# Kernel optimization log

Hardware: AMD Instinct MI355X
Metric: run time of the kernel (lower is better)

The kernel has to match this reference:

```python
import jax, jax.numpy as jnp
import numpy as np

SCALE_H = 160.0
SCALE_W = 160.0
ALIGNED = False


def setup_inputs() -> dict:
    key = jax.random.key(0)
    k1, k2, k3, k4 = jax.random.split(key, 4)
    N, C, H, W, K = 8, 256, 160, 160, 1024
    feat = jax.random.normal(k1, (N, C, H, W), dtype=jnp.float32)
    b = jax.random.randint(k2, (K,), 0, N).astype(jnp.float32)
    xs = jnp.sort(jax.random.uniform(k3, (K, 2), dtype=jnp.float32), axis=1)
    ys = jnp.sort(jax.random.uniform(k4, (K, 2), dtype=jnp.float32), axis=1)
    rois = jnp.stack([b, xs[:, 0], ys[:, 0], xs[:, 1], ys[:, 1]], axis=1)
    return {"input_feature_map": feat, "rois": rois,
            "output_height": 14, "output_width": 14}


def _roi_align(feat, rois, output_height, output_width):
    N, C, H, W = feat.shape
    K = rois.shape[0]
    b = rois[:, 0].astype(jnp.int32)
    x1 = rois[:, 1] * SCALE_W
    y1 = rois[:, 2] * SCALE_H
    x2 = rois[:, 3] * SCALE_W
    y2 = rois[:, 4] * SCALE_H
    # normalized [0,1] grid over the ROI interior
    gx = jnp.linspace(0.0, 1.0, output_width, dtype=feat.dtype)
    gy = jnp.linspace(0.0, 1.0, output_height, dtype=feat.dtype)
    fx = x1[:, None, None] + gx[None, None, :] * (x2 - x1)[:, None, None]  # (K,1,Wo)
    fy = y1[:, None, None] + gy[None, :, None] * (y2 - y1)[:, None, None]  # (K,Ho,1)
    # convert to grid_sample normalized coords, then back to pixel coords
    if ALIGNED:
        ngx = fx / (W - 1) * 2 - 1
        ngy = fy / (H - 1) * 2 - 1
        ix = (ngx + 1) * 0.5 * (W - 1)
        iy = (ngy + 1) * 0.5 * (H - 1)
    else:
        ngx = fx / W * 2 - 1
        ngy = fy / H * 2 - 1
        ix = ((ngx + 1) * W - 1) * 0.5
        iy = ((ngy + 1) * H - 1) * 0.5
    x0 = jnp.floor(ix).astype(jnp.int32)
    y0 = jnp.floor(iy).astype(jnp.int32)
    x1i = x0 + 1
    y1i = y0 + 1
    wx1 = ix - x0.astype(feat.dtype)
    wx0 = 1.0 - wx1
    wy1 = iy - y0.astype(feat.dtype)
    wy0 = 1.0 - wy1
    # zeros padding: out-of-bounds corners contribute 0
    vx0 = ((x0 >= 0) & (x0 < W)).astype(feat.dtype)
    vx1 = ((x1i >= 0) & (x1i < W)).astype(feat.dtype)
    vy0 = ((y0 >= 0) & (y0 < H)).astype(feat.dtype)
    vy1 = ((y1i >= 0) & (y1i < H)).astype(feat.dtype)
    x0c = jnp.clip(x0, 0, W - 1)
    x1c = jnp.clip(x1i, 0, W - 1)
    y0c = jnp.clip(y0, 0, H - 1)
    y1c = jnp.clip(y1i, 0, H - 1)
    # flat gather table: (N*H*W, C) -- no per-ROI feature-map duplication
    featf = jnp.transpose(feat, (0, 2, 3, 1)).reshape(N * H * W, C)
    bb = b[:, None, None]  # (K,1,1)

    def corner(yy, xx, w):
        lin = (bb * H + yy) * W + xx  # broadcast -> (K,Ho,Wo)
        lin = jnp.broadcast_to(lin, (K, output_height, output_width))
        v = featf[lin.reshape(-1)].reshape(K, output_height, output_width, C)
        w = jnp.broadcast_to(w, (K, output_height, output_width))
        return v * w[..., None]

    out = (corner(y0c, x0c, wy0 * wx0 * vy0 * vx0)
           + corner(y0c, x1c, wy0 * wx1 * vy0 * vx1)
           + corner(y1c, x0c, wy1 * wx0 * vy1 * vx0)
           + corner(y1c, x1c, wy1 * wx1 * vy1 * vx1))
    return jnp.transpose(out, (0, 3, 1, 2))  # (K, C, Ho, Wo)


def reference(input_feature_map, rois, output_height, output_width):
    return _roi_align(input_feature_map, rois, int(output_height), int(output_width))
```

## Files before the change

### kernel.cpp

```cpp
#include <hip/hip_runtime.h>
#include <hip/hip_fp16.h>


#define FM_N 8
#define FM_C 256
#define FM_H 160
#define FM_W 160
#define PLANE (FM_H * FM_W)
#define PLANE4 (PLANE / 4)
#define OH 14
#define OW 14
#define OSP (OH * OW)
#define KMAX 1024
#define SCALE_HW 160.0f
#define MAIN_BLK 1024
#define ROWS 81
#define LDSW 164
#define ROW_F4 (FM_W / 4)
#define PL_PIX (ROWS * LDSW)
#define PL_F4 (ROWS * ROW_F4)
#define FRONTPAD 2
#define TAILPAD 6

typedef float f4 __attribute__((ext_vector_type(4)));

#define WS_KINFO_OFF 32
#define WS_SAMPLES_BYTE_OFF 12544

__device__ __forceinline__ float iy_of(float y1, float y2, int oy) {
  return fmaf((float)oy * (1.0f / (OH - 1)), y2 - y1, y1) - 0.5f;
}

__global__ __launch_bounds__(1024) void setup_kernel(
    const float* __restrict__ rois, int K, int* __restrict__ ws) {
  __shared__ int cnt[16];
  __shared__ int soff[16];
  const int t = threadIdx.x;
  if (t < 16) cnt[t] = 0;
  __syncthreads();
  int posA = 0, posB = 0, c0 = 0, b = 0;
  if (t < K) {
    b = (int)rois[t * 5];
    const float y1 = rois[t * 5 + 2] * SCALE_HW;
    const float y2 = rois[t * 5 + 4] * SCALE_HW;
#pragma unroll
    for (int oy = 0; oy < OH; ++oy)
      c0 += (iy_of(y1, y2, oy) < 80.0f) ? 1 : 0;
    posA = atomicAdd(&cnt[b * 2 + 0], c0 * OW);
    posB = atomicAdd(&cnt[b * 2 + 1], (OH - c0) * OW);
  }
  __syncthreads();
  if (t == 0) {
    int acc = 0;
    for (int i = 0; i < 16; ++i) { soff[i] = acc; acc += cnt[i]; }
  }
  __syncthreads();
  if (t < 16) { ws[t] = cnt[t]; ws[16 + t] = soff[t]; }
  if (t < K) {
    ws[WS_KINFO_OFF + 3 * t + 0] = soff[b * 2 + 0] + posA;
    ws[WS_KINFO_OFF + 3 * t + 1] = soff[b * 2 + 1] + posB;
    ws[WS_KINFO_OFF + 3 * t + 2] = c0;
  }
}

__global__ __launch_bounds__(256) void precompute_kernel(
    const float* __restrict__ rois, const int* __restrict__ ws, int total,
    uint4* __restrict__ samples) {
  const int g = blockIdx.x * 256 + threadIdx.x;
  if (g >= total) return;
  const int k = g / OSP;
  const int s = g - k * OSP;
  const int oy = s / OW;
  const int ox = s - oy * OW;

  const float x1 = rois[k * 5 + 1] * SCALE_HW;
  const float y1 = rois[k * 5 + 2] * SCALE_HW;
  const float x2 = rois[k * 5 + 3] * SCALE_HW;
  const float y2 = rois[k * 5 + 4] * SCALE_HW;

  const float ix = fmaf((float)ox * (1.0f / (OW - 1)), x2 - x1, x1) - 0.5f;
  const float iy = iy_of(y1, y2, oy);

  const float fx0 = floorf(ix);
  const float fy0 = floorf(iy);
  const int x0 = (int)fx0;
  const int y0 = (int)fy0;
  const float wx1 = ix - fx0;
  const float wy1 = iy - fy0;

  const bool vx0 = (x0 >= 0 && x0 < FM_W);
  const bool vx1 = (x0 + 1 >= 0 && x0 + 1 < FM_W);
  const unsigned vy0 = (y0 >= 0 && y0 < FM_H) ? 1u : 0u;
  const unsigned vy1 = (y0 + 1 >= 0 && y0 + 1 < FM_H) ? 1u : 0u;

  const int x0c = min(max(x0, 0), FM_W - 1);
  const int x1c = min(max(x0 + 1, 0), FM_W - 1);
  const int y0c = min(max(y0, 0), FM_H - 1);
  const int y1c = min(max(y0 + 1, 0), FM_H - 1);

  const int ca = ws[WS_KINFO_OFF + 3 * k + 0];
  const int cb = ws[WS_KINFO_OFF + 3 * k + 1];
  const int c0 = ws[WS_KINFO_OFF + 3 * k + 2];
  const int h = (oy >= c0) ? 1 : 0;
  const int row0 = h ? 79 : 0;

  const int yl0 = y0c - row0;
  const int o00 = yl0 * LDSW + x0c;
  const int o01 = yl0 * LDSW + x1c;
  const int bx = vx1 ? (o01 - 1) : o00;
  const unsigned bxs = (unsigned)(bx + FRONTPAD);
  const unsigned dyr = (unsigned)(y1c - y0c);
  unsigned wq = (unsigned)(wy1 * 8192.0f + 0.5f);
  wq = wq > 8191u ? 8191u : wq;

  const __half2 axh = __floats2half2_rn((1.0f - wx1) * (vx0 ? 1.0f : 0.0f),
                                        wx1 * (vx1 ? 1.0f : 0.0f));
  uint4 sd;
  sd.x = bxs | (dyr << 15) | (wq << 16) | (vy0 << 29) | (vy1 << 30);
  sd.y = *(const unsigned*)&axh;
  sd.z = (unsigned)(k * (FM_C * OSP) + s);
  sd.w = 0;

  const int pos = h ? (cb + (oy - c0) * OW + ox) : (ca + oy * OW + ox);
  samples[pos] = sd;
}

__global__ __launch_bounds__(MAIN_BLK) void roi_align_main_kernel(
    const float* __restrict__ feat, const int* __restrict__ ws,
    const uint4* __restrict__ samples, float* __restrict__ out) {
  __shared__ __align__(16) uint2 planeBuf[FRONTPAD + PL_PIX + TAILPAD];

  const int q = blockIdx.x;
  const int b = blockIdx.y;
  const int h = blockIdx.z;
  const int t = threadIdx.x;
  const int row0 = h ? 79 : 0;
  const int c0ch = 4 * q;

  const int scount = ws[b * 2 + h];
  const int soff = ws[16 + b * 2 + h];
  const uint4* __restrict__ stream = samples + soff;

  const uint2 zz = {0u, 0u};
  if (t < FRONTPAD) planeBuf[t] = zz;
  if (t < TAILPAD) planeBuf[FRONTPAD + PL_PIX + t] = zz;
  if (t < ROWS * 4) {
    const int y = t >> 2;
    planeBuf[FRONTPAD + y * LDSW + FM_W + (t & 3)] = zz;
  }

  {
    const f4* __restrict__ s0 =
        (const f4*)(feat + ((size_t)b * FM_C + c0ch) * PLANE) + row0 * ROW_F4;
    const f4* __restrict__ s1 = s0 + PLANE4;
    const f4* __restrict__ s2 = s0 + 2 * PLANE4;
    const f4* __restrict__ s3 = s0 + 3 * PLANE4;
    for (int i = t; i < PL_F4; i += MAIN_BLK) {
      const f4 a = __builtin_nontemporal_load(&s0[i]);
      const f4 bb = __builtin_nontemporal_load(&s1[i]);
      const f4 c = __builtin_nontemporal_load(&s2[i]);
      const f4 d = __builtin_nontemporal_load(&s3[i]);
      const int y = (int)((unsigned)i / ROW_F4);
      const int j = i - y * ROW_F4;
      const __half2 p0l = __floats2half2_rn(a.x, bb.x);
      const __half2 p0h = __floats2half2_rn(c.x, d.x);
      const __half2 p1l = __floats2half2_rn(a.y, bb.y);
      const __half2 p1h = __floats2half2_rn(c.y, d.y);
      const __half2 p2l = __floats2half2_rn(a.z, bb.z);
      const __half2 p2h = __floats2half2_rn(c.z, d.z);
      const __half2 p3l = __floats2half2_rn(a.w, bb.w);
      const __half2 p3h = __floats2half2_rn(c.w, d.w);
      uint4 u01, u23;
      u01.x = *(const unsigned*)&p0l;
      u01.y = *(const unsigned*)&p0h;
      u01.z = *(const unsigned*)&p1l;
      u01.w = *(const unsigned*)&p1h;
      u23.x = *(const unsigned*)&p2l;
      u23.y = *(const unsigned*)&p2h;
      u23.z = *(const unsigned*)&p3l;
      u23.w = *(const unsigned*)&p3h;
      uint4* __restrict__ dst =
          (uint4*)&planeBuf[FRONTPAD + y * LDSW + 4 * j];
      dst[0] = u01;
      dst[1] = u23;
    }
  }
  __syncthreads();

  const uint2* __restrict__ pb = planeBuf;
  float* __restrict__ outc = out + (size_t)c0ch * OSP;
#pragma unroll 2
  for (int w = t; w < scount; w += MAIN_BLK) {
    const uint4 sd = stream[w];
    const int bxs = (int)(sd.x & 0x7FFFu);
    const int o10 = bxs + (int)((sd.x >> 15) & 1u) * LDSW;

    const uint2 L0 = pb[bxs];
    const uint2 R0 = pb[bxs + 1];
    const uint2 L1 = pb[o10];
    const uint2 R1 = pb[o10 + 1];

    const __half2 ax = *(const __half2*)&sd.y;
    const __half2 axl = __half2half2(__low2half(ax));
    const __half2 axr = __half2half2(__high2half(ax));

    const __half2 hx0l = __hfma2(*(const __half2*)&R0.x, axr,
                                 __hmul2(*(const __half2*)&L0.x, axl));
    const __half2 hx0h = __hfma2(*(const __half2*)&R0.y, axr,
                                 __hmul2(*(const __half2*)&L0.y, axl));
    const __half2 hx1l = __hfma2(*(const __half2*)&R1.x, axr,
                                 __hmul2(*(const __half2*)&L1.x, axl));
    const __half2 hx1h = __hfma2(*(const __half2*)&R1.y, axr,
                                 __hmul2(*(const __half2*)&L1.y, axl));

    const float wy1 = (float)((sd.x >> 16) & 0x1FFFu) * (1.0f / 8192.0f);
    const float ay0 = ((sd.x >> 29) & 1u) ? (1.0f - wy1) : 0.0f;
    const float ay1 = ((sd.x >> 30) & 1u) ? wy1 : 0.0f;

    const float vA = ay0 * __low2float(hx0l) + ay1 * __low2float(hx1l);
    const float vB = ay0 * __high2float(hx0l) + ay1 * __high2float(hx1l);
    const float vC = ay0 * __low2float(hx0h) + ay1 * __low2float(hx1h);
    const float vD = ay0 * __high2float(hx0h) + ay1 * __high2float(hx1h);

    float* __restrict__ dst = outc + sd.z;
    dst[0] = vA;
    dst[OSP] = vB;
    dst[2 * OSP] = vC;
    dst[3 * OSP] = vD;
  }
}

extern "C" void kernel_launch(void* const* d_in, const int* in_sizes, int n_in,
                              void* d_out, int out_size, void* d_ws, size_t ws_size,
                              hipStream_t stream) {
  const float* feat = (const float*)d_in[0];
  const float* rois = (const float*)d_in[1];
  float* out = (float*)d_out;
  int* ws = (int*)d_ws;
  uint4* samples = (uint4*)((char*)d_ws + WS_SAMPLES_BYTE_OFF);

  const int K = in_sizes[1] / 5;
  const int total = K * OSP;

  setup_kernel<<<1, 1024, 0, stream>>>(rois, K, ws);
  precompute_kernel<<<(total + 255) / 256, 256, 0, stream>>>(rois, ws, total,
                                                             samples);
  roi_align_main_kernel<<<dim3(FM_C / 4, FM_N, 2), MAIN_BLK, 0, stream>>>(
      feat, ws, samples, out);
}
```

Before: 91.24 us.

## Tile feature map into row quarters with eight channels per block

Measured after the change: 97.67 us. +7.0%, slower.

```diff
diff --git a/kernel.cpp b/kernel.cpp
--- a/kernel.cpp
+++ b/kernel.cpp
@@ -14,52 +14,67 @@
 #define KMAX 1024
 #define SCALE_HW 160.0f
 #define MAIN_BLK 1024
-#define ROWS 81
+#define QROWS 40
+#define ROWS 41
 #define LDSW 164
 #define ROW_F4 (FM_W / 4)
 #define PL_PIX (ROWS * LDSW)
-#define PL_F4 (ROWS * ROW_F4)
-#define FRONTPAD 2
-#define TAILPAD 6
+#define FRONTPAD 1
+#define TAILPAD 4
 
 typedef float f4 __attribute__((ext_vector_type(4)));
 
-#define WS_KINFO_OFF 32
-#define WS_SAMPLES_BYTE_OFF 12544
+#define WS_KINFO_OFF 64
+#define WS_SAMPLES_BYTE_OFF 33024
 
 __device__ __forceinline__ float iy_of(float y1, float y2, int oy) {
   return fmaf((float)oy * (1.0f / (OH - 1)), y2 - y1, y1) - 0.5f;
 }
 
+__device__ __forceinline__ int quarter_of(float y1, float y2, int oy) {
+  const int y0 = (int)floorf(iy_of(y1, y2, oy));
+  const int y0c = min(max(y0, 0), FM_H - 1);
+  return y0c / QROWS;
+}
+
 __global__ __launch_bounds__(1024) void setup_kernel(
     const float* __restrict__ rois, int K, int* __restrict__ ws) {
-  __shared__ int cnt[16];
-  __shared__ int soff[16];
+  __shared__ int cnt[32];
+  __shared__ int soff[32];
   const int t = threadIdx.x;
-  if (t < 16) cnt[t] = 0;
-  __syncthreads();
-  int posA = 0, posB = 0, c0 = 0, b = 0;
+  if (t < 32) cnt[t] = 0;
+  __syncthreads();
+  int n[4] = {0, 0, 0, 0};
+  int st[4] = {0, 0, 0, 0};
+  int pos[4] = {0, 0, 0, 0};
+  int b = 0;
   if (t < K) {
     b = (int)rois[t * 5];
     const float y1 = rois[t * 5 + 2] * SCALE_HW;
     const float y2 = rois[t * 5 + 4] * SCALE_HW;
 #pragma unroll
-    for (int oy = 0; oy < OH; ++oy)
-      c0 += (iy_of(y1, y2, oy) < 80.0f) ? 1 : 0;
-    posA = atomicAdd(&cnt[b * 2 + 0], c0 * OW);
-    posB = atomicAdd(&cnt[b * 2 + 1], (OH - c0) * OW);
+    for (int oy = 0; oy < OH; ++oy) {
+      const int q = quarter_of(y1, y2, oy);
+      if (n[q] == 0) st[q] = oy;
+      n[q]++;
+    }
+#pragma unroll
+    for (int q = 0; q < 4; ++q)
+      if (n[q]) pos[q] = atomicAdd(&cnt[b * 4 + q], n[q] * OW);
   }
   __syncthreads();
   if (t == 0) {
     int acc = 0;
-    for (int i = 0; i < 16; ++i) { soff[i] = acc; acc += cnt[i]; }
-  }
-  __syncthreads();
-  if (t < 16) { ws[t] = cnt[t]; ws[16 + t] = soff[t]; }
+    for (int i = 0; i < 32; ++i) { soff[i] = acc; acc += cnt[i]; }
+  }
+  __syncthreads();
+  if (t < 32) { ws[t] = cnt[t]; ws[32 + t] = soff[t]; }
   if (t < K) {
-    ws[WS_KINFO_OFF + 3 * t + 0] = soff[b * 2 + 0] + posA;
-    ws[WS_KINFO_OFF + 3 * t + 1] = soff[b * 2 + 1] + posB;
-    ws[WS_KINFO_OFF + 3 * t + 2] = c0;
+#pragma unroll
+    for (int q = 0; q < 4; ++q) {
+      ws[WS_KINFO_OFF + 8 * t + q] = soff[b * 4 + q] + pos[q];
+      ws[WS_KINFO_OFF + 8 * t + 4 + q] = st[q];
+    }
   }
 }
 
@@ -98,11 +113,8 @@
   const int y0c = min(max(y0, 0), FM_H - 1);
   const int y1c = min(max(y0 + 1, 0), FM_H - 1);
 
-  const int ca = ws[WS_KINFO_OFF + 3 * k + 0];
-  const int cb = ws[WS_KINFO_OFF + 3 * k + 1];
-  const int c0 = ws[WS_KINFO_OFF + 3 * k + 2];
-  const int h = (oy >= c0) ? 1 : 0;
-  const int row0 = h ? 79 : 0;
+  const int q = y0c / QROWS;
+  const int row0 = q * QROWS;
 
   const int yl0 = y0c - row0;
   const int o00 = yl0 * LDSW + x0c;
@@ -121,27 +133,28 @@
   sd.z = (unsigned)(k * (FM_C * OSP) + s);
   sd.w = 0;
 
-  const int pos = h ? (cb + (oy - c0) * OW + ox) : (ca + oy * OW + ox);
-  samples[pos] = sd;
+  const int coff = ws[WS_KINFO_OFF + 8 * k + q];
+  const int stq = ws[WS_KINFO_OFF + 8 * k + 4 + q];
+  samples[coff + (oy - stq) * OW + ox] = sd;
 }
 
 __global__ __launch_bounds__(MAIN_BLK) void roi_align_main_kernel(
     const float* __restrict__ feat, const int* __restrict__ ws,
     const uint4* __restrict__ samples, float* __restrict__ out) {
-  __shared__ __align__(16) uint2 planeBuf[FRONTPAD + PL_PIX + TAILPAD];
-
-  const int q = blockIdx.x;
+  __shared__ __align__(16) uint4 planeBuf[FRONTPAD + PL_PIX + TAILPAD];
+
+  const int o8 = blockIdx.x;
   const int b = blockIdx.y;
-  const int h = blockIdx.z;
+  const int q = blockIdx.z;
   const int t = threadIdx.x;
-  const int row0 = h ? 79 : 0;
-  const int c0ch = 4 * q;
-
-  const int scount = ws[b * 2 + h];
-  const int soff = ws[16 + b * 2 + h];
+  const int row0 = q * QROWS;
+  const int c0ch = 8 * o8;
+
+  const int scount = ws[b * 4 + q];
+  const int soff = ws[32 + b * 4 + q];
   const uint4* __restrict__ stream = samples + soff;
 
-  const uint2 zz = {0u, 0u};
+  const uint4 zz = {0u, 0u, 0u, 0u};
   if (t < FRONTPAD) planeBuf[t] = zz;
   if (t < TAILPAD) planeBuf[FRONTPAD + PL_PIX + t] = zz;
   if (t < ROWS * 4) {
@@ -150,44 +163,36 @@
   }
 
   {
-    const f4* __restrict__ s0 =
-        (const f4*)(feat + ((size_t)b * FM_C + c0ch) * PLANE) + row0 * ROW_F4;
-    const f4* __restrict__ s1 = s0 + PLANE4;
-    const f4* __restrict__ s2 = s0 + 2 * PLANE4;
-    const f4* __restrict__ s3 = s0 + 3 * PLANE4;
-    for (int i = t; i < PL_F4; i += MAIN_BLK) {
-      const f4 a = __builtin_nontemporal_load(&s0[i]);
-      const f4 bb = __builtin_nontemporal_load(&s1[i]);
-      const f4 c = __builtin_nontemporal_load(&s2[i]);
-      const f4 d = __builtin_nontemporal_load(&s3[i]);
+    const f4* __restrict__ sp =
+        (const f4*)(feat + ((size_t)b * FM_C + c0ch) * PLANE);
+    for (int i = t; i < ROWS * ROW_F4; i += MAIN_BLK) {
       const int y = (int)((unsigned)i / ROW_F4);
       const int j = i - y * ROW_F4;
-      const __half2 p0l = __floats2half2_rn(a.x, bb.x);
-      const __half2 p0h = __floats2half2_rn(c.x, d.x);
-      const __half2 p1l = __floats2half2_rn(a.y, bb.y);
-      const __half2 p1h = __floats2half2_rn(c.y, d.y);
-      const __half2 p2l = __floats2half2_rn(a.z, bb.z);
-      const __half2 p2h = __floats2half2_rn(c.z, d.z);
-      const __half2 p3l = __floats2half2_rn(a.w, bb.w);
-      const __half2 p3h = __floats2half2_rn(c.w, d.w);
-      uint4 u01, u23;
-      u01.x = *(const unsigned*)&p0l;
-      u01.y = *(const unsigned*)&p0h;
-      u01.z = *(const unsigned*)&p1l;
-      u01.w = *(const unsigned*)&p1h;
-      u23.x = *(const unsigned*)&p2l;
-      u23.y = *(const unsigned*)&p2h;
-      u23.z = *(const unsigned*)&p3l;
-      u23.w = *(const unsigned*)&p3h;
-      uint4* __restrict__ dst =
-          (uint4*)&planeBuf[FRONTPAD + y * LDSW + 4 * j];
-      dst[0] = u01;
-      dst[1] = u23;
+      const int srow = min(row0 + y, FM_H - 1);
+      const int so = srow * ROW_F4 + j;
+      f4 v[8];
+#pragma unroll
+      for (int c = 0; c < 8; ++c)
+        v[c] = __builtin_nontemporal_load(&sp[c * PLANE4 + so]);
+      uint4* __restrict__ dst = &planeBuf[FRONTPAD + y * LDSW + 4 * j];
+#pragma unroll
+      for (int e = 0; e < 4; ++e) {
+        const __half2 a0 = __floats2half2_rn(v[0][e], v[1][e]);
+        const __half2 a1 = __floats2half2_rn(v[2][e], v[3][e]);
+        const __half2 a2 = __floats2half2_rn(v[4][e], v[5][e]);
+        const __half2 a3 = __floats2half2_rn(v[6][e], v[7][e]);
+        uint4 u;
+        u.x = *(const unsigned*)&a0;
+        u.y = *(const unsigned*)&a1;
+        u.z = *(const unsigned*)&a2;
+        u.w = *(const unsigned*)&a3;
+        dst[e] = u;
+      }
     }
   }
   __syncthreads();
 
-  const uint2* __restrict__ pb = planeBuf;
+  const uint4* __restrict__ pb = planeBuf;
   float* __restrict__ outc = out + (size_t)c0ch * OSP;
 #pragma unroll 2
   for (int w = t; w < scount; w += MAIN_BLK) {
@@ -195,38 +200,45 @@
     const int bxs = (int)(sd.x & 0x7FFFu);
     const int o10 = bxs + (int)((sd.x >> 15) & 1u) * LDSW;
 
-    const uint2 L0 = pb[bxs];
-    const uint2 R0 = pb[bxs + 1];
-    const uint2 L1 = pb[o10];
-    const uint2 R1 = pb[o10 + 1];
+    const uint4 L0 = pb[bxs];
+    const uint4 R0 = pb[bxs + 1];
+    const uint4 L1 = pb[o10];
+    const uint4 R1 = pb[o10 + 1];
 
     const __half2 ax = *(const __half2*)&sd.y;
     const __half2 axl = __half2half2(__low2half(ax));
     const __half2 axr = __half2half2(__high2half(ax));
 
-    const __half2 hx0l = __hfma2(*(const __half2*)&R0.x, axr,
-                                 __hmul2(*(const __half2*)&L0.x, axl));
-    const __half2 hx0h = __hfma2(*(const __half2*)&R0.y, axr,
-                                 __hmul2(*(const __half2*)&L0.y, axl));
-    const __half2 hx1l = __hfma2(*(const __half2*)&R1.x, axr,
-                                 __hmul2(*(const __half2*)&L1.x, axl));
-    const __half2 hx1h = __hfma2(*(const __half2*)&R1.y, axr,
-                                 __hmul2(*(const __half2*)&L1.y, axl));
+    const __half2 h0a = __hfma2(*(const __half2*)&R0.x, axr,
+                                __hmul2(*(const __half2*)&L0.x, axl));
+    const __half2 h0b = __hfma2(*(const __half2*)&R0.y, axr,
+                                __hmul2(*(const __half2*)&L0.y, axl));
+    const __half2 h0c = __hfma2(*(const __half2*)&R0.z, axr,
+                                __hmul2(*(const __half2*)&L0.z, axl));
+    const __half2 h0d = __hfma2(*(const __half2*)&R0.w, axr,
+                                __hmul2(*(const __half2*)&L0.w, axl));
+    const __half2 h1a = __hfma2(*(const __half2*)&R1.x, axr,
+                                __hmul2(*(const __half2*)&L1.x, axl));
+    const __half2 h1b = __hfma2(*(const __half2*)&R1.y, axr,
+                                __hmul2(*(const __half2*)&L1.y, axl));
+    const __half2 h1c = __hfma2(*(const __half2*)&R1.z, axr,
+                                __hmul2(*(const __half2*)&L1.z, axl));
+    const __half2 h1d = __hfma2(*(const __half2*)&R1.w, axr,
+                                __hmul2(*(const __half2*)&L1.w, axl));
 
     const float wy1 = (float)((sd.x >> 16) & 0x1FFFu) * (1.0f / 8192.0f);
     const float ay0 = ((sd.x >> 29) & 1u) ? (1.0f - wy1) : 0.0f;
     const float ay1 = ((sd.x >> 30) & 1u) ? wy1 : 0.0f;
 
-    const float vA = ay0 * __low2float(hx0l) + ay1 * __low2float(hx1l);
-    const float vB = ay0 * __high2float(hx0l) + ay1 * __high2float(hx1l);
-    const float vC = ay0 * __low2float(hx0h) + ay1 * __low2float(hx1h);
-    const float vD = ay0 * __high2float(hx0h) + ay1 * __high2float(hx1h);
-
     float* __restrict__ dst = outc + sd.z;
-    dst[0] = vA;
-    dst[OSP] = vB;
-    dst[2 * OSP] = vC;
-    dst[3 * OSP] = vD;
+    dst[0 * OSP] = ay0 * __low2float(h0a) + ay1 * __low2float(h1a);
+    dst[1 * OSP] = ay0 * __high2float(h0a) + ay1 * __high2float(h1a);
+    dst[2 * OSP] = ay0 * __low2float(h0b) + ay1 * __low2float(h1b);
+    dst[3 * OSP] = ay0 * __high2float(h0b) + ay1 * __high2float(h1b);
+    dst[4 * OSP] = ay0 * __low2float(h0c) + ay1 * __low2float(h1c);
+    dst[5 * OSP] = ay0 * __high2float(h0c) + ay1 * __high2float(h1c);
+    dst[6 * OSP] = ay0 * __low2float(h0d) + ay1 * __low2float(h1d);
+    dst[7 * OSP] = ay0 * __high2float(h0d) + ay1 * __high2float(h1d);
   }
 }
 
@@ -245,6 +257,6 @@
   setup_kernel<<<1, 1024, 0, stream>>>(rois, K, ws);
   precompute_kernel<<<(total + 255) / 256, 256, 0, stream>>>(rois, ws, total,
                                                              samples);
-  roi_align_main_kernel<<<dim3(FM_C / 4, FM_N, 2), MAIN_BLK, 0, stream>>>(
+  roi_align_main_kernel<<<dim3(FM_C / 8, FM_N, 4), MAIN_BLK, 0, stream>>>(
       feat, ws, samples, out);
 }
```

## Split feature plane into four row bands to shrink LDS tile and raise occupancy

Applied to the files above, without the earlier changes.

Result: slower. 95.86 us (+5.1%).

```diff
diff --git a/kernel.cpp b/kernel.cpp
--- a/kernel.cpp
+++ b/kernel.cpp
@@ -14,52 +14,67 @@
 #define KMAX 1024
 #define SCALE_HW 160.0f
 #define MAIN_BLK 1024
-#define ROWS 81
+#define QROWS 40
+#define ROWS 41
 #define LDSW 164
 #define ROW_F4 (FM_W / 4)
 #define PL_PIX (ROWS * LDSW)
-#define PL_F4 (ROWS * ROW_F4)
 #define FRONTPAD 2
 #define TAILPAD 6
 
 typedef float f4 __attribute__((ext_vector_type(4)));
 
-#define WS_KINFO_OFF 32
-#define WS_SAMPLES_BYTE_OFF 12544
+#define WS_KINFO_OFF 64
+#define WS_SAMPLES_BYTE_OFF 33024
 
 __device__ __forceinline__ float iy_of(float y1, float y2, int oy) {
   return fmaf((float)oy * (1.0f / (OH - 1)), y2 - y1, y1) - 0.5f;
 }
 
+__device__ __forceinline__ int quarter_of(float y1, float y2, int oy) {
+  const int y0 = (int)floorf(iy_of(y1, y2, oy));
+  const int y0c = min(max(y0, 0), FM_H - 1);
+  return y0c / QROWS;
+}
+
 __global__ __launch_bounds__(1024) void setup_kernel(
     const float* __restrict__ rois, int K, int* __restrict__ ws) {
-  __shared__ int cnt[16];
-  __shared__ int soff[16];
+  __shared__ int cnt[32];
+  __shared__ int soff[32];
   const int t = threadIdx.x;
-  if (t < 16) cnt[t] = 0;
-  __syncthreads();
-  int posA = 0, posB = 0, c0 = 0, b = 0;
+  if (t < 32) cnt[t] = 0;
+  __syncthreads();
+  int n[4] = {0, 0, 0, 0};
+  int st[4] = {0, 0, 0, 0};
+  int pos[4] = {0, 0, 0, 0};
+  int b = 0;
   if (t < K) {
     b = (int)rois[t * 5];
     const float y1 = rois[t * 5 + 2] * SCALE_HW;
     const float y2 = rois[t * 5 + 4] * SCALE_HW;
 #pragma unroll
-    for (int oy = 0; oy < OH; ++oy)
-      c0 += (iy_of(y1, y2, oy) < 80.0f) ? 1 : 0;
-    posA = atomicAdd(&cnt[b * 2 + 0], c0 * OW);
-    posB = atomicAdd(&cnt[b * 2 + 1], (OH - c0) * OW);
+    for (int oy = 0; oy < OH; ++oy) {
+      const int q = quarter_of(y1, y2, oy);
+      if (n[q] == 0) st[q] = oy;
+      n[q]++;
+    }
+#pragma unroll
+    for (int q = 0; q < 4; ++q)
+      if (n[q]) pos[q] = atomicAdd(&cnt[b * 4 + q], n[q] * OW);
   }
   __syncthreads();
   if (t == 0) {
     int acc = 0;
-    for (int i = 0; i < 16; ++i) { soff[i] = acc; acc += cnt[i]; }
-  }
-  __syncthreads();
-  if (t < 16) { ws[t] = cnt[t]; ws[16 + t] = soff[t]; }
+    for (int i = 0; i < 32; ++i) { soff[i] = acc; acc += cnt[i]; }
+  }
+  __syncthreads();
+  if (t < 32) { ws[t] = cnt[t]; ws[32 + t] = soff[t]; }
   if (t < K) {
-    ws[WS_KINFO_OFF + 3 * t + 0] = soff[b * 2 + 0] + posA;
-    ws[WS_KINFO_OFF + 3 * t + 1] = soff[b * 2 + 1] + posB;
-    ws[WS_KINFO_OFF + 3 * t + 2] = c0;
+#pragma unroll
+    for (int q = 0; q < 4; ++q) {
+      ws[WS_KINFO_OFF + 8 * t + q] = soff[b * 4 + q] + pos[q];
+      ws[WS_KINFO_OFF + 8 * t + 4 + q] = st[q];
+    }
   }
 }
 
@@ -98,11 +113,8 @@
   const int y0c = min(max(y0, 0), FM_H - 1);
   const int y1c = min(max(y0 + 1, 0), FM_H - 1);
 
-  const int ca = ws[WS_KINFO_OFF + 3 * k + 0];
-  const int cb = ws[WS_KINFO_OFF + 3 * k + 1];
-  const int c0 = ws[WS_KINFO_OFF + 3 * k + 2];
-  const int h = (oy >= c0) ? 1 : 0;
-  const int row0 = h ? 79 : 0;
+  const int q = y0c / QROWS;
+  const int row0 = q * QROWS;
 
   const int yl0 = y0c - row0;
   const int o00 = yl0 * LDSW + x0c;
@@ -121,24 +133,25 @@
   sd.z = (unsigned)(k * (FM_C * OSP) + s);
   sd.w = 0;
 
-  const int pos = h ? (cb + (oy - c0) * OW + ox) : (ca + oy * OW + ox);
-  samples[pos] = sd;
-}
-
-__global__ __launch_bounds__(MAIN_BLK) void roi_align_main_kernel(
+  const int coff = ws[WS_KINFO_OFF + 8 * k + q];
+  const int stq = ws[WS_KINFO_OFF + 8 * k + 4 + q];
+  samples[coff + (oy - stq) * OW + ox] = sd;
+}
+
+__global__ __launch_bounds__(MAIN_BLK, 8) void roi_align_main_kernel(
     const float* __restrict__ feat, const int* __restrict__ ws,
     const uint4* __restrict__ samples, float* __restrict__ out) {
   __shared__ __align__(16) uint2 planeBuf[FRONTPAD + PL_PIX + TAILPAD];
 
-  const int q = blockIdx.x;
+  const int qd = blockIdx.x;
   const int b = blockIdx.y;
-  const int h = blockIdx.z;
+  const int q = blockIdx.z;
   const int t = threadIdx.x;
-  const int row0 = h ? 79 : 0;
-  const int c0ch = 4 * q;
-
-  const int scount = ws[b * 2 + h];
-  const int soff = ws[16 + b * 2 + h];
+  const int row0 = q * QROWS;
+  const int c0ch = 4 * qd;
+
+  const int scount = ws[b * 4 + q];
+  const int soff = ws[32 + b * 4 + q];
   const uint4* __restrict__ stream = samples + soff;
 
   const uint2 zz = {0u, 0u};
@@ -151,17 +164,19 @@
 
   {
     const f4* __restrict__ s0 =
-        (const f4*)(feat + ((size_t)b * FM_C + c0ch) * PLANE) + row0 * ROW_F4;
+        (const f4*)(feat + ((size_t)b * FM_C + c0ch) * PLANE);
     const f4* __restrict__ s1 = s0 + PLANE4;
     const f4* __restrict__ s2 = s0 + 2 * PLANE4;
     const f4* __restrict__ s3 = s0 + 3 * PLANE4;
-    for (int i = t; i < PL_F4; i += MAIN_BLK) {
-      const f4 a = __builtin_nontemporal_load(&s0[i]);
-      const f4 bb = __builtin_nontemporal_load(&s1[i]);
-      const f4 c = __builtin_nontemporal_load(&s2[i]);
-      const f4 d = __builtin_nontemporal_load(&s3[i]);
+    for (int i = t; i < ROWS * ROW_F4; i += MAIN_BLK) {
       const int y = (int)((unsigned)i / ROW_F4);
       const int j = i - y * ROW_F4;
+      const int srow = min(row0 + y, FM_H - 1);
+      const int so = srow * ROW_F4 + j;
+      const f4 a = __builtin_nontemporal_load(&s0[so]);
+      const f4 bb = __builtin_nontemporal_load(&s1[so]);
+      const f4 c = __builtin_nontemporal_load(&s2[so]);
+      const f4 d = __builtin_nontemporal_load(&s3[so]);
       const __half2 p0l = __floats2half2_rn(a.x, bb.x);
       const __half2 p0h = __floats2half2_rn(c.x, d.x);
       const __half2 p1l = __floats2half2_rn(a.y, bb.y);
@@ -245,6 +260,6 @@
   setup_kernel<<<1, 1024, 0, stream>>>(rois, K, ws);
   precompute_kernel<<<(total + 255) / 256, 256, 0, stream>>>(rois, ws, total,
                                                              samples);
-  roi_align_main_kernel<<<dim3(FM_C / 4, FM_N, 2), MAIN_BLK, 0, stream>>>(
+  roi_align_main_kernel<<<dim3(FM_C / 4, FM_N, 4), MAIN_BLK, 0, stream>>>(
       feat, ws, samples, out);
 }
```
